# Kernel optimization log

Measured on AMD Instinct MI355X. Metric: run time of the kernel, lower is better.

The kernel has to match this reference:

```python
import jax, jax.numpy as jnp
import numpy as np

N_NODES = 10000
N_EDGES = 320000
IN_FEATS = 256
NUM_HEADS = 8
OUT_FEATS = 64
NEG_SLOPE = 0.2


def setup_inputs() -> dict:
    key = jax.random.key(0)
    k = jax.random.split(key, 7)
    feat = jax.random.normal(k[0], (N_NODES, IN_FEATS), dtype=jnp.float32)
    W = jax.random.normal(k[1], (IN_FEATS, NUM_HEADS * OUT_FEATS), dtype=jnp.float32) * (1.0 / np.sqrt(IN_FEATS))
    attn_l = jax.random.normal(k[2], (1, NUM_HEADS, OUT_FEATS), dtype=jnp.float32) * 0.1
    attn_r = jax.random.normal(k[3], (1, NUM_HEADS, OUT_FEATS), dtype=jnp.float32) * 0.1
    adj = jax.random.uniform(k[4], (N_NODES, N_NODES), dtype=jnp.float32)
    src = jax.random.randint(k[5], (N_EDGES,), 0, N_NODES, dtype=jnp.int32)
    dst = jax.random.randint(k[6], (N_EDGES,), 0, N_NODES, dtype=jnp.int32)
    return {"feat": feat, "W": W, "attn_l": attn_l, "attn_r": attn_r,
            "adj": adj, "src": src, "dst": dst, "idx": 0}


def reference(feat, W, attn_l, attn_r, adj, src, dst, idx):
    N = feat.shape[0]
    # node projection: [N, H, D]
    ft = (feat @ W).reshape(N, NUM_HEADS, OUT_FEATS)
    # per-node attention logits [N, H]
    el = jnp.sum(ft * attn_l, axis=-1)
    er = jnp.sum(ft * attn_r, axis=-1)
    # u_add_v on edges + LeakyReLU -> [E, H]
    e = el[src] + er[dst]
    e = jnp.where(e > 0, e, NEG_SLOPE * e)
    # edge softmax: segment softmax over destination node
    m = jax.ops.segment_max(e, dst, num_segments=N)          # [N, H]
    ex = jnp.exp(e - m[dst])                                  # [E, H]
    s = jax.ops.segment_sum(ex, dst, num_segments=N)          # [N, H]
    a = ex / s[dst]                                           # [E, H]
    # vectorized adjacency masking (replaces per-edge Python loop)
    a = a * adj[src + idx, dst + idx][:, None]                # [E, H]
    # u_mul_e + scatter-sum aggregation -> [N, H, D]
    msg = ft[src] * a[:, :, None]                             # [E, H, D]
    rst = jax.ops.segment_sum(msg, dst, num_segments=N)
    return rst
```

## Files before the change

kernel.cpp:

```cpp
#include <hip/hip_runtime.h>
#include <hip/hip_bf16.h>
#include <cstdint>
#include <cstddef>

#define IN_FEATS 256
#define NUM_HEADS 8
#define HD 512
#define CH 32
#define ELLCAP 128

typedef __attribute__((ext_vector_type(8))) short bf16x8;
typedef __attribute__((ext_vector_type(4))) float f32x4;

__device__ inline unsigned short bf16_bits(float f) {
    unsigned x = __float_as_uint(f);
    x += 0x7fffu + ((x >> 16) & 1u);
    return (unsigned short)(x >> 16);
}


__global__ __launch_bounds__(256) void k0_kernel(const float* __restrict__ W,
                                                 const float* __restrict__ al,
                                                 const float* __restrict__ ar,
                                                 int* __restrict__ deg,
                                                 float* __restrict__ wlr,
                                                 unsigned short* __restrict__ Wt,
                                                 int M) {
    const int b = blockIdx.x;
    const int t = threadIdx.x;
    if (b < 40) {
        int i = b * 256 + t;
        if (i < M) deg[i] = 0;
        return;
    }
    if (b < 72) {
        __shared__ float tile[64][65];
        const int bb = b - 40;
        const int h = bb >> 2;
        const int k0 = (bb & 3) * 64;
#pragma unroll 4
        for (int it = 0; it < 16; ++it) {
            int r = it * 4 + (t >> 6);
            int c = t & 63;
            tile[r][c] = W[(size_t)(k0 + r) * HD + h * 64 + c];
        }
        __syncthreads();
#pragma unroll 4
        for (int it = 0; it < 16; ++it) {
            int c = it * 4 + (t >> 6);
            int k = t & 63;
            Wt[((size_t)h * 64 + c) * IN_FEATS + k0 + k] = bf16_bits(tile[k][c]);
        }
        return;
    }
    const int k = (b - 72) * 4 + (t >> 6);
    const int l = t & 63;
    float4 w0 = *(const float4*)(W + (size_t)k * HD + 8 * l);
    float4 w1 = *(const float4*)(W + (size_t)k * HD + 8 * l + 4);
    float4 a0 = *(const float4*)(al + 8 * l);
    float4 a1 = *(const float4*)(al + 8 * l + 4);
    float4 b0 = *(const float4*)(ar + 8 * l);
    float4 b1 = *(const float4*)(ar + 8 * l + 4);
    float pl = w0.x * a0.x + w0.y * a0.y + w0.z * a0.z + w0.w * a0.w +
               w1.x * a1.x + w1.y * a1.y + w1.z * a1.z + w1.w * a1.w;
    float pr = w0.x * b0.x + w0.y * b0.y + w0.z * b0.z + w0.w * b0.w +
               w1.x * b1.x + w1.y * b1.y + w1.z * b1.z + w1.w * b1.w;
#pragma unroll
    for (int off = 1; off < 8; off <<= 1) {
        pl += __shfl_xor(pl, off);
        pr += __shfl_xor(pr, off);
    }
    if ((l & 7) == 0) {
        wlr[k * 16 + (l >> 3)] = pl;
        wlr[k * 16 + 8 + (l >> 3)] = pr;
    }
}


__global__ __launch_bounds__(256) void k1_kernel(const int* __restrict__ src,
                                                 const int* __restrict__ dst,
                                                 int* __restrict__ deg,
                                                 int* __restrict__ ell,
                                                 const float* __restrict__ feat,
                                                 const float* __restrict__ wlr,
                                                 const unsigned short* __restrict__ Wt,
                                                 float* __restrict__ el,
                                                 float* __restrict__ er,
                                                 signed char* __restrict__ ftq,
                                                 float* __restrict__ scaleb,
                                                 int E, int M, int nb_sc, int nb_elr) {
    const int b = blockIdx.x;
    const int t = threadIdx.x;
    if (b < nb_sc) {
        int i = b * 256 + t;
        if (i < E) {
            int d = dst[i];
            int r = atomicAdd(&deg[d], 1);
            if (r < ELLCAP) ell[(size_t)d * ELLCAP + r] = src[i];
        }
        return;
    }
    if (b < nb_sc + nb_elr) {
        __shared__ float wle[256][17];
        for (int i = t; i < 256 * 16; i += 256) wle[i >> 4][i & 15] = wlr[i];
        __syncthreads();
        const int lane = t & 63, wv = t >> 6;
        const int n = (b - nb_sc) * 4 + wv;
        if (n >= M) return;
        const float* frow = feat + (size_t)n * IN_FEATS;
        float p[16];
#pragma unroll
        for (int h = 0; h < 16; ++h) p[h] = 0.f;
#pragma unroll
        for (int j = 0; j < 4; ++j) {
            int k = lane + 64 * j;
            float fv = frow[k];
#pragma unroll
            for (int h = 0; h < 16; ++h) p[h] = fmaf(fv, wle[k][h], p[h]);
        }
        float outv = 0.f;
#pragma unroll
        for (int h = 0; h < 16; ++h) {
            float v = p[h];
#pragma unroll
            for (int off = 32; off; off >>= 1) v += __shfl_xor(v, off);
            outv = (lane == h) ? v : outv;
        }
        if (lane < 8) el[n * NUM_HEADS + lane] = outv;
        else if (lane < 16) er[n * NUM_HEADS + lane - 8] = outv;
        return;
    }
    {
        const int id = b - nb_sc - nb_elr;
        const int NBX = (M + 63) / 64;
        const int bx = id % NBX;
        const int by = id / NBX;
        const int lane = t & 63, wv = t >> 6;
        const int n0 = bx * 64 + wv * 16;
        const int r = lane & 15;
        const int kg = lane >> 4;
        const int arow = min(n0 + r, M - 1);
        const float* aptr = feat + (size_t)arow * IN_FEATS + kg * 8;
        const short* bptr = (const short*)Wt + ((size_t)by * 64 + r) * IN_FEATS + kg * 8;
        f32x4 acc[4];
#pragma unroll
        for (int c = 0; c < 4; ++c) acc[c] = (f32x4){0.f, 0.f, 0.f, 0.f};
#pragma unroll
        for (int kk = 0; kk < IN_FEATS; kk += 32) {
            float4 a0 = *(const float4*)(aptr + kk);
            float4 a1 = *(const float4*)(aptr + kk + 4);
            bf16x8 a;
            unsigned short* ap = (unsigned short*)&a;
            ap[0] = bf16_bits(a0.x); ap[1] = bf16_bits(a0.y);
            ap[2] = bf16_bits(a0.z); ap[3] = bf16_bits(a0.w);
            ap[4] = bf16_bits(a1.x); ap[5] = bf16_bits(a1.y);
            ap[6] = bf16_bits(a1.z); ap[7] = bf16_bits(a1.w);
#pragma unroll
            for (int c = 0; c < 4; ++c) {
                bf16x8 bb = *(const bf16x8*)(bptr + (size_t)c * 16 * IN_FEATS + kk);
                acc[c] = __builtin_amdgcn_mfma_f32_16x16x32_bf16(a, bb, acc[c], 0, 0, 0);
            }
        }
        float iscale[4], sc[4];
#pragma unroll
        for (int i = 0; i < 4; ++i) {
            float m = fmaxf(fmaxf(fabsf(acc[0][i]), fabsf(acc[1][i])),
                            fmaxf(fabsf(acc[2][i]), fabsf(acc[3][i])));
#pragma unroll
            for (int off = 1; off < 16; off <<= 1) m = fmaxf(m, __shfl_xor(m, off));
            sc[i] = m * (1.0f / 127.0f);
            iscale[i] = (m > 1e-30f) ? (127.0f / m) : 0.f;
        }
        const int orow0 = n0 + kg * 4;
        if (r == 0) {
#pragma unroll
            for (int i = 0; i < 4; ++i) {
                int rr = orow0 + i;
                if (rr < M) scaleb[rr * NUM_HEADS + by] = sc[i];
            }
        }
#pragma unroll
        for (int c = 0; c < 4; ++c) {
#pragma unroll
            for (int i = 0; i < 4; ++i) {
                int rr = orow0 + i;
                if (rr < M) {
                    int q = __float2int_rn(acc[c][i] * iscale[i]);
                    q = max(-127, min(127, q));
                    ftq[(size_t)rr * HD + by * 64 + c * 16 + r] = (signed char)q;
                }
            }
        }
    }
}


__global__ __launch_bounds__(256) void agg_kernel(
    const signed char* __restrict__ ftq, const float* __restrict__ scaleb,
    const float* __restrict__ el, const float* __restrict__ er,
    const float* __restrict__ adj, const int* __restrict__ deg,
    const int* __restrict__ ell, const int* __restrict__ idxp,
    float* __restrict__ out, int M) {
    const int n = blockIdx.x;
    const int t = threadIdx.x;
    const int h = t >> 5;
    const int cnt = min(deg[n], ELLCAP);
    if (cnt == 0) {
        *(float2*)(out + (size_t)n * HD + 2 * t) = make_float2(0.f, 0.f);
        return;
    }
    const int idx = idxp[0];
    const int hh = t & 7;
    const int j0 = t >> 3;
    const float er_hh = er[n * NUM_HEADS + hh];
    const float* adj_col = adj + (size_t)idx * M + (n + idx);
    const int* erow = ell + (size_t)n * ELLCAP;

    __shared__ float w_lds[2][CH][8];
    __shared__ int s_lds[2][CH];
    __shared__ float red[256];
    __shared__ float inv_s[8];

    float ssum = 0.f;
    float2 acc = make_float2(0.f, 0.f);

    int s_r = 0;
    float w_r = 0.f;
    auto stage = [&](int base) {
        int j = base + j0;
        if (j < cnt) {
            s_r = erow[j];
            float e = el[s_r * NUM_HEADS + hh] + er_hh;
            e = (e > 0.f) ? e : 0.2f * e;
            float pv = __expf(e);
            ssum += pv;
            w_r = pv * adj_col[(size_t)s_r * M] * scaleb[s_r * NUM_HEADS + hh];
        }
    };
    auto write_lds = [&](int buf, int base) {
        int j = base + j0;
        if (j < cnt) {
            w_lds[buf][j0][hh] = w_r;
            if (hh == 0) s_lds[buf][j0] = s_r;
        }
    };

    int buf = 0;
    stage(0);
    write_lds(0, 0);
    __syncthreads();
    for (int base = 0; base < cnt; base += CH) {
        const bool more = (base + CH) < cnt;
        if (more) stage(base + CH);
        int c = min(CH, cnt - base);
        const int* srow = &s_lds[buf][0];
        const float* wrow = &w_lds[buf][0][0];
#pragma unroll 4
        for (int jj = 0; jj < c; ++jj) {
            int s = srow[jj];
            unsigned short v = *(const unsigned short*)(ftq + (size_t)s * HD + 2 * t);
            float fx = (float)(signed char)(v & 0xff);
            float fy = (float)(signed char)(v >> 8);
            float w = wrow[jj * 8 + h];
            acc.x = fmaf(w, fx, acc.x);
            acc.y = fmaf(w, fy, acc.y);
        }
        if (more) {
            write_lds(buf ^ 1, base + CH);
            __syncthreads();
            buf ^= 1;
        }
    }
    red[t] = ssum;
    __syncthreads();
#pragma unroll
    for (int off = 128; off >= 8; off >>= 1) {
        if (t < off) red[t] += red[t + off];
        __syncthreads();
    }
    if (t < 8) inv_s[t] = 1.f / red[t];
    __syncthreads();
    const float inv = inv_s[h];
    *(float2*)(out + (size_t)n * HD + 2 * t) = make_float2(acc.x * inv, acc.y * inv);
}


extern "C" void kernel_launch(void* const* d_in, const int* in_sizes, int n_in,
                              void* d_out, int out_size, void* d_ws, size_t ws_size,
                              hipStream_t stream) {
    const float* feat   = (const float*)d_in[0];
    const float* W      = (const float*)d_in[1];
    const float* attn_l = (const float*)d_in[2];
    const float* attn_r = (const float*)d_in[3];
    const float* adj    = (const float*)d_in[4];
    const int*   src    = (const int*)d_in[5];
    const int*   dst    = (const int*)d_in[6];
    const int*   idxp   = (const int*)d_in[7];
    float* out = (float*)d_out;

    const int M = in_sizes[0] / IN_FEATS;
    const int E = in_sizes[5];

    char* ws = (char*)d_ws;
    size_t off = 0;
    auto alloc = [&](size_t bytes) -> void* {
        off = (off + 255) & ~(size_t)255;
        void* p = ws + off;
        off += bytes;
        return p;
    };
    signed char* ftq    = (signed char*)alloc((size_t)M * HD);
    float* scaleb       = (float*)alloc((size_t)M * NUM_HEADS * sizeof(float));
    unsigned short* Wt  = (unsigned short*)alloc((size_t)HD * IN_FEATS * sizeof(short));
    float* wlr       = (float*)alloc((size_t)IN_FEATS * 16 * sizeof(float));
    float* el        = (float*)alloc((size_t)M * NUM_HEADS * sizeof(float));
    float* er        = (float*)alloc((size_t)M * NUM_HEADS * sizeof(float));
    int*   deg       = (int*)alloc((size_t)M * sizeof(int));
    int*   ell       = (int*)alloc((size_t)M * ELLCAP * sizeof(int));

    k0_kernel<<<136, 256, 0, stream>>>(W, attn_l, attn_r, deg, wlr, Wt, M);

    const int nb_sc = (E + 255) / 256;
    const int nb_elr = (M + 3) / 4;
    const int NBX = (M + 63) / 64;
    const int nb_ft = NBX * NUM_HEADS;
    k1_kernel<<<nb_sc + nb_elr + nb_ft, 256, 0, stream>>>(src, dst, deg, ell,
                                                          feat, wlr, Wt, el, er,
                                                          ftq, scaleb,
                                                          E, M, nb_sc, nb_elr);

    agg_kernel<<<M, 256, 0, stream>>>(ftq, scaleb, el, er, adj, deg, ell, idxp, out, M);
}
```

Measured before the change: 109.2 us.

## Compute attention logits el/er in the MFMA projection epilogue

```diff
diff --git a/kernel.cpp b/kernel.cpp
--- a/kernel.cpp
+++ b/kernel.cpp
@@ -20,10 +20,7 @@
 
 
 __global__ __launch_bounds__(256) void k0_kernel(const float* __restrict__ W,
-                                                 const float* __restrict__ al,
-                                                 const float* __restrict__ ar,
                                                  int* __restrict__ deg,
-                                                 float* __restrict__ wlr,
                                                  unsigned short* __restrict__ Wt,
                                                  int M) {
     const int b = blockIdx.x;
@@ -33,46 +30,22 @@
         if (i < M) deg[i] = 0;
         return;
     }
-    if (b < 72) {
-        __shared__ float tile[64][65];
-        const int bb = b - 40;
-        const int h = bb >> 2;
-        const int k0 = (bb & 3) * 64;
+    __shared__ float tile[64][65];
+    const int bb = b - 40;
+    const int h = bb >> 2;
+    const int k0 = (bb & 3) * 64;
 #pragma unroll 4
-        for (int it = 0; it < 16; ++it) {
-            int r = it * 4 + (t >> 6);
-            int c = t & 63;
-            tile[r][c] = W[(size_t)(k0 + r) * HD + h * 64 + c];
-        }
-        __syncthreads();
+    for (int it = 0; it < 16; ++it) {
+        int r = it * 4 + (t >> 6);
+        int c = t & 63;
+        tile[r][c] = W[(size_t)(k0 + r) * HD + h * 64 + c];
+    }
+    __syncthreads();
 #pragma unroll 4
-        for (int it = 0; it < 16; ++it) {
-            int c = it * 4 + (t >> 6);
-            int k = t & 63;
-            Wt[((size_t)h * 64 + c) * IN_FEATS + k0 + k] = bf16_bits(tile[k][c]);
-        }
-        return;
-    }
-    const int k = (b - 72) * 4 + (t >> 6);
-    const int l = t & 63;
-    float4 w0 = *(const float4*)(W + (size_t)k * HD + 8 * l);
-    float4 w1 = *(const float4*)(W + (size_t)k * HD + 8 * l + 4);
-    float4 a0 = *(const float4*)(al + 8 * l);
-    float4 a1 = *(const float4*)(al + 8 * l + 4);
-    float4 b0 = *(const float4*)(ar + 8 * l);
-    float4 b1 = *(const float4*)(ar + 8 * l + 4);
-    float pl = w0.x * a0.x + w0.y * a0.y + w0.z * a0.z + w0.w * a0.w +
-               w1.x * a1.x + w1.y * a1.y + w1.z * a1.z + w1.w * a1.w;
-    float pr = w0.x * b0.x + w0.y * b0.y + w0.z * b0.z + w0.w * b0.w +
-               w1.x * b1.x + w1.y * b1.y + w1.z * b1.z + w1.w * b1.w;
-#pragma unroll
-    for (int off = 1; off < 8; off <<= 1) {
-        pl += __shfl_xor(pl, off);
-        pr += __shfl_xor(pr, off);
-    }
-    if ((l & 7) == 0) {
-        wlr[k * 16 + (l >> 3)] = pl;
-        wlr[k * 16 + 8 + (l >> 3)] = pr;
+    for (int it = 0; it < 16; ++it) {
+        int c = it * 4 + (t >> 6);
+        int k = t & 63;
+        Wt[((size_t)h * 64 + c) * IN_FEATS + k0 + k] = bf16_bits(tile[k][c]);
     }
 }
 
@@ -82,13 +55,14 @@
                                                  int* __restrict__ deg,
                                                  int* __restrict__ ell,
                                                  const float* __restrict__ feat,
-                                                 const float* __restrict__ wlr,
+                                                 const float* __restrict__ al,
+                                                 const float* __restrict__ ar,
                                                  const unsigned short* __restrict__ Wt,
                                                  float* __restrict__ el,
                                                  float* __restrict__ er,
                                                  signed char* __restrict__ ftq,
                                                  float* __restrict__ scaleb,
-                                                 int E, int M, int nb_sc, int nb_elr) {
+                                                 int E, int M, int nb_sc) {
     const int b = blockIdx.x;
     const int t = threadIdx.x;
     if (b < nb_sc) {
@@ -100,38 +74,8 @@
         }
         return;
     }
-    if (b < nb_sc + nb_elr) {
-        __shared__ float wle[256][17];
-        for (int i = t; i < 256 * 16; i += 256) wle[i >> 4][i & 15] = wlr[i];
-        __syncthreads();
-        const int lane = t & 63, wv = t >> 6;
-        const int n = (b - nb_sc) * 4 + wv;
-        if (n >= M) return;
-        const float* frow = feat + (size_t)n * IN_FEATS;
-        float p[16];
-#pragma unroll
-        for (int h = 0; h < 16; ++h) p[h] = 0.f;
-#pragma unroll
-        for (int j = 0; j < 4; ++j) {
-            int k = lane + 64 * j;
-            float fv = frow[k];
-#pragma unroll
-            for (int h = 0; h < 16; ++h) p[h] = fmaf(fv, wle[k][h], p[h]);
-        }
-        float outv = 0.f;
-#pragma unroll
-        for (int h = 0; h < 16; ++h) {
-            float v = p[h];
-#pragma unroll
-            for (int off = 32; off; off >>= 1) v += __shfl_xor(v, off);
-            outv = (lane == h) ? v : outv;
-        }
-        if (lane < 8) el[n * NUM_HEADS + lane] = outv;
-        else if (lane < 16) er[n * NUM_HEADS + lane - 8] = outv;
-        return;
-    }
     {
-        const int id = b - nb_sc - nb_elr;
+        const int id = b - nb_sc;
         const int NBX = (M + 63) / 64;
         const int bx = id % NBX;
         const int by = id / NBX;
@@ -161,22 +105,42 @@
                 acc[c] = __builtin_amdgcn_mfma_f32_16x16x32_bf16(a, bb, acc[c], 0, 0, 0);
             }
         }
-        float iscale[4], sc[4];
+        float alv[4], arv[4];
+#pragma unroll
+        for (int c = 0; c < 4; ++c) {
+            alv[c] = al[by * 64 + c * 16 + r];
+            arv[c] = ar[by * 64 + c * 16 + r];
+        }
+        float iscale[4], sc[4], pl[4], pr[4];
 #pragma unroll
         for (int i = 0; i < 4; ++i) {
             float m = fmaxf(fmaxf(fabsf(acc[0][i]), fabsf(acc[1][i])),
                             fmaxf(fabsf(acc[2][i]), fabsf(acc[3][i])));
-#pragma unroll
-            for (int off = 1; off < 16; off <<= 1) m = fmaxf(m, __shfl_xor(m, off));
+            float l = acc[0][i] * alv[0] + acc[1][i] * alv[1] +
+                      acc[2][i] * alv[2] + acc[3][i] * alv[3];
+            float q = acc[0][i] * arv[0] + acc[1][i] * arv[1] +
+                      acc[2][i] * arv[2] + acc[3][i] * arv[3];
+#pragma unroll
+            for (int off = 1; off < 16; off <<= 1) {
+                m = fmaxf(m, __shfl_xor(m, off));
+                l += __shfl_xor(l, off);
+                q += __shfl_xor(q, off);
+            }
             sc[i] = m * (1.0f / 127.0f);
             iscale[i] = (m > 1e-30f) ? (127.0f / m) : 0.f;
+            pl[i] = l;
+            pr[i] = q;
         }
         const int orow0 = n0 + kg * 4;
         if (r == 0) {
 #pragma unroll
             for (int i = 0; i < 4; ++i) {
                 int rr = orow0 + i;
-                if (rr < M) scaleb[rr * NUM_HEADS + by] = sc[i];
+                if (rr < M) {
+                    scaleb[rr * NUM_HEADS + by] = sc[i];
+                    el[rr * NUM_HEADS + by] = pl[i];
+                    er[rr * NUM_HEADS + by] = pr[i];
+                }
             }
         }
 #pragma unroll
@@ -312,22 +276,19 @@
     signed char* ftq    = (signed char*)alloc((size_t)M * HD);
     float* scaleb       = (float*)alloc((size_t)M * NUM_HEADS * sizeof(float));
     unsigned short* Wt  = (unsigned short*)alloc((size_t)HD * IN_FEATS * sizeof(short));
-    float* wlr       = (float*)alloc((size_t)IN_FEATS * 16 * sizeof(float));
     float* el        = (float*)alloc((size_t)M * NUM_HEADS * sizeof(float));
     float* er        = (float*)alloc((size_t)M * NUM_HEADS * sizeof(float));
     int*   deg       = (int*)alloc((size_t)M * sizeof(int));
     int*   ell       = (int*)alloc((size_t)M * ELLCAP * sizeof(int));
 
-    k0_kernel<<<136, 256, 0, stream>>>(W, attn_l, attn_r, deg, wlr, Wt, M);
+    k0_kernel<<<72, 256, 0, stream>>>(W, deg, Wt, M);
 
     const int nb_sc = (E + 255) / 256;
-    const int nb_elr = (M + 3) / 4;
     const int NBX = (M + 63) / 64;
     const int nb_ft = NBX * NUM_HEADS;
-    k1_kernel<<<nb_sc + nb_elr + nb_ft, 256, 0, stream>>>(src, dst, deg, ell,
-                                                          feat, wlr, Wt, el, er,
-                                                          ftq, scaleb,
-                                                          E, M, nb_sc, nb_elr);
+    k1_kernel<<<nb_sc + nb_ft, 256, 0, stream>>>(src, dst, deg, ell,
+                                                 feat, attn_l, attn_r, Wt, el, er,
+                                                 ftq, scaleb, E, M, nb_sc);
 
     agg_kernel<<<M, 256, 0, stream>>>(ftq, scaleb, el, er, adj, deg, ell, idxp, out, M);
 }
```

After: 100.2 us. 1.09x faster.
